# Kernel tuning notes

Hardware: AMD Instinct MI355X
Metric: run time of the kernel (lower is better)

## Reference

```python
import jax, jax.numpy as jnp
import numpy as np

N_NODES = 100000
EPS = 1e-5


def setup_inputs() -> dict:
    key = jax.random.key(0)
    ks = jax.random.split(key, 16)
    E_half = 1_600_000
    s = jax.random.randint(ks[0], (E_half,), 0, N_NODES, dtype=jnp.int32)
    d = jax.random.randint(ks[1], (E_half,), 0, N_NODES, dtype=jnp.int32)
    # bidirected graph, like dgl.to_bidirected
    src = jnp.concatenate([s, d])
    dst = jnp.concatenate([d, s])

    def glorot(k, i, o):
        lim = np.sqrt(6.0 / (i + o)).astype(np.float32)
        return jax.random.uniform(k, (i, o), jnp.float32, -lim, lim)

    return {
        "x": jax.random.normal(ks[2], (N_NODES, 128), jnp.float32),
        "src": src,
        "dst": dst,
        "W1": glorot(ks[3], 128, 256), "b1": jnp.zeros((256,), jnp.float32),
        "gamma1": jnp.ones((256,), jnp.float32), "beta1": jnp.zeros((256,), jnp.float32),
        "W2": glorot(ks[4], 256, 256), "b2": jnp.zeros((256,), jnp.float32),
        "gamma2": jnp.ones((256,), jnp.float32), "beta2": jnp.zeros((256,), jnp.float32),
        "W3": glorot(ks[5], 256, 40), "b3": jnp.zeros((40,), jnp.float32),
    }


def _graph_conv(x, src, dst, norm, W, b):
    # DGL GraphConv norm='both': h = D^{-1/2} A D^{-1/2} (x) W + b
    # project first when it shrinks the feature dim (matches DGL's ordering trick)
    if W.shape[0] > W.shape[1]:
        x = x @ W
        h = x * norm[:, None]
        m = jax.ops.segment_sum(h[src], dst, num_segments=N_NODES)
        return m * norm[:, None] + b
    h = x * norm[:, None]
    m = jax.ops.segment_sum(h[src], dst, num_segments=N_NODES)
    return (m * norm[:, None]) @ W + b


def _bn(h, gamma, beta):
    # BatchNorm1d in training mode: batch statistics over nodes, biased variance
    mean = jnp.mean(h, axis=0)
    var = jnp.var(h, axis=0)
    return (h - mean) * jax.lax.rsqrt(var + EPS) * gamma + beta


def reference(x, src, dst, W1, b1, gamma1, beta1, W2, b2, gamma2, beta2, W3, b3):
    # symmetric degrees (graph is bidirected), clamp min 1 like DGL
    deg = jax.ops.segment_sum(jnp.ones_like(dst, dtype=jnp.float32), dst,
                              num_segments=N_NODES)
    norm = jax.lax.rsqrt(jnp.maximum(deg, 1.0))

    h = _graph_conv(x, src, dst, norm, W1, b1)
    h = jax.nn.relu(_bn(h, gamma1, beta1))
    h = _graph_conv(h, src, dst, norm, W2, b2)
    h = jax.nn.relu(_bn(h, gamma2, beta2))
    h = _graph_conv(h, src, dst, norm, W3, b3)
    return jax.nn.log_softmax(h, axis=-1)
```

## Files before the change

kernel.cpp:

```cpp
#include <hip/hip_runtime.h>
#include <cstdint>
#include <cstddef>

#define NN 100000
#define BN_EPS 1e-5f

#define NB_SHIFT 7
#define NBUCK ((NN >> NB_SHIFT) + 1)
#define BSLOT 6400
#define T1_EPT 16
#define T1_TILE (256*T1_EPT)

typedef __attribute__((ext_vector_type(8))) short short8;
typedef __attribute__((ext_vector_type(4))) float f32x4;
typedef __attribute__((ext_vector_type(2))) float f32x2;

static __device__ __forceinline__ float bflo(unsigned u){ return __uint_as_float(u<<16); }
static __device__ __forceinline__ float bfhi(unsigned u){ return __uint_as_float(u & 0xFFFF0000u); }
static __device__ __forceinline__ unsigned short f2bf(float f){
  unsigned u = __float_as_uint(f);
  u += 0x7FFFu + ((u>>16)&1u);
  return (unsigned short)(u>>16);
}
static __device__ __forceinline__ unsigned pk2(float a, float b){
  return (unsigned)f2bf(a) | ((unsigned)f2bf(b) << 16);
}


__global__ __launch_bounds__(256) void k_b1(const int* __restrict__ src,
    const int* __restrict__ dst, int* __restrict__ bcnt,
    int* __restrict__ epairs, int E){
  __shared__ int hist[NBUCK];
  int tid = threadIdx.x;
  for(int j=tid; j<NBUCK; j+=256) hist[j]=0;
  __syncthreads();
  int base = blockIdx.x*T1_TILE;
  int pk[T1_EPT], bk[T1_EPT], r[T1_EPT];
  #pragma unroll
  for(int i=0;i<T1_EPT;i++){
    int e = base + i*256 + tid;
    if(e<E){
      int s=src[e], d=dst[e];
      bk[i]=d>>NB_SHIFT;
      pk[i]= s | ((d&127)<<20);
      r[i]=atomicAdd(&hist[bk[i]], 1);
    }
  }
  __syncthreads();
  for(int j=tid; j<NBUCK; j+=256){
    int h = hist[j];
    if(h>0) hist[j] = atomicAdd(&bcnt[j*16], h);
  }
  __syncthreads();
  #pragma unroll
  for(int i=0;i<T1_EPT;i++){
    int e = base + i*256 + tid;
    if(e<E) epairs[(size_t)bk[i]*BSLOT + hist[bk[i]] + r[i]] = pk[i];
  }
}

__global__ __launch_bounds__(256) void k_b2a(const int* __restrict__ epairs,
    const int* __restrict__ bcnt, float* __restrict__ norm, int* __restrict__ deg,
    int* __restrict__ ptot){
  __shared__ int h[128];
  int b = blockIdx.x, tid = threadIdx.x;
  if(tid<128) h[tid]=0;
  __syncthreads();
  int c = bcnt[b*16];
  const int* ep = epairs + (size_t)b*BSLOT;
  for(int j=tid; j<c; j+=256) atomicAdd(&h[ep[j]>>20], 1);
  __syncthreads();
  int n0 = b<<NB_SHIFT, nmax = min(128, NN-n0);
  if(tid<nmax){
    norm[n0+tid] = rsqrtf(fmaxf((float)h[tid], 1.0f));
    deg[n0+tid] = h[tid];
  }
  if(tid<64){
    int p0=(h[2*tid]+7)&~7, p1=(h[2*tid+1]+7)&~7;
    int s=p0+p1;
    #pragma unroll
    for(int off=1; off<64; off<<=1) s += __shfl_xor(s, off, 64);
    if(tid==0) ptot[b]=s;
  }
}

__global__ __launch_bounds__(1024) void k_scanB(const int* __restrict__ ptot,
    int* __restrict__ bbase, int* __restrict__ rp, float* __restrict__ norm){
  __shared__ int sm[1024];
  int t = threadIdx.x;
  int v = (t<NBUCK)? ptot[t] : 0;
  sm[t]=v; __syncthreads();
  for(int off=1; off<1024; off<<=1){
    int u = (t>=off)? sm[t-off] : 0;
    __syncthreads();
    sm[t]+=u;
    __syncthreads();
  }
  if(t<NBUCK) bbase[t] = sm[t]-v;
  if(t==NBUCK-1){ bbase[NBUCK]=sm[t]; rp[NN]=sm[t]; }
  if(t==0) norm[NN]=0.f;
}

__global__ __launch_bounds__(256) void k_b2b(const int* __restrict__ epairs,
    const int* __restrict__ bcnt, const int* __restrict__ bbase,
    const int* __restrict__ deg, int* __restrict__ rp, int* __restrict__ esrc){
  __shared__ int h[128];
  __shared__ int loc[129];
  int b = blockIdx.x, tid = threadIdx.x;
  int n0 = b<<NB_SHIFT, nmax = min(128, NN-n0);
  if(tid<128) h[tid] = (tid<nmax) ? deg[n0+tid] : 0;
  __syncthreads();
  if(tid<64){
    int p0=(h[2*tid]+7)&~7, p1=(h[2*tid+1]+7)&~7;
    int s=p0+p1;
    #pragma unroll
    for(int off=1; off<64; off<<=1){ int u=__shfl_up(s, off, 64); if(tid>=off) s+=u; }
    loc[2*tid]   = s-p0-p1;
    loc[2*tid+1] = s-p1;
    if(tid==63) loc[128]=s;
  }
  __syncthreads();
  int base = bbase[b];
  if(tid<nmax) rp[n0+tid] = base + loc[tid];
  if(tid<128) h[tid] = base + loc[tid];
  __syncthreads();
  int c = bcnt[b*16];
  const int* ep = epairs + (size_t)b*BSLOT;
  for(int j=tid; j<c; j+=256){
    int p = ep[j];
    int pos = atomicAdd(&h[p>>20], 1);
    esrc[pos] = p & 0xFFFFF;
  }
  __syncthreads();
  for(int i=tid; i<nmax; i+=256){
    int end = base + loc[i+1];
    for(int j=h[i]; j<end; j++) esrc[j]=NN;
  }
}

#define PB_W1 1
#define PB_W2 129
#define PB_W3 385
#define PB_SX 449
#define PB_END (PB_SX + 6250)

__global__ __launch_bounds__(256) void k_prep(
    const float* __restrict__ W1, const float* __restrict__ W2, const float* __restrict__ W3,
    const float* __restrict__ x, const float* __restrict__ norm,
    unsigned short* __restrict__ Wt1, unsigned short* __restrict__ Wt2,
    unsigned short* __restrict__ Wt3, unsigned char* __restrict__ Hx8,
    unsigned short* __restrict__ X3p, unsigned short* __restrict__ Z){
  int bid = blockIdx.x, t = threadIdx.x;
  if(bid == 0){
    if(t<128) Hx8[(size_t)NN*128 + t] = 0;
    if(t<40)  X3p[(size_t)NN*64 + t] = 0;
    Z[(size_t)NN*256 + t] = 0;
  }else if(bid < PB_W2){
    int i = (bid-PB_W1)*256 + t;
    int k = i >> 8, n = i & 255;
    Wt1[(size_t)n*128 + k] = f2bf(W1[i]);
  }else if(bid < PB_W3){
    int i = (bid-PB_W2)*256 + t;
    int k = i >> 8, n = i & 255;
    Wt2[(size_t)n*256 + k] = f2bf(W2[i]);
  }else if(bid < PB_SX){
    int i = (bid-PB_W3)*256 + t;
    int n = i >> 8, k = i & 255;
    Wt3[i] = (n < 40) ? f2bf(W3[(size_t)k*40 + n]) : (unsigned short)0;
  }else{
    int i = (bid-PB_SX)*256 + t;
    float4 v0 = *(const float4*)(x + (size_t)i*8);
    float4 v1 = *(const float4*)(x + (size_t)i*8 + 4);
    float nn = norm[i>>4];
    int p0 = __builtin_amdgcn_cvt_pk_fp8_f32(v0.x*nn, v0.y*nn, 0, false);
    p0     = __builtin_amdgcn_cvt_pk_fp8_f32(v0.z*nn, v0.w*nn, p0, true);
    int p1 = __builtin_amdgcn_cvt_pk_fp8_f32(v1.x*nn, v1.y*nn, 0, false);
    p1     = __builtin_amdgcn_cvt_pk_fp8_f32(v1.z*nn, v1.w*nn, p1, true);
    uint2 w; w.x = (unsigned)p0; w.y = (unsigned)p1;
    *(uint2*)(Hx8 + (size_t)i*8) = w;
  }
}


__global__ __launch_bounds__(256) void k_bnrelu8(const unsigned short* __restrict__ Z,
    const float* __restrict__ sums, const float* __restrict__ gamma,
    const float* __restrict__ beta, const float* __restrict__ norm,
    unsigned char* __restrict__ H8, int total4){
  __shared__ float s_sc[256], s_sh[256];
  int t = threadIdx.x;
  {
    float mean = sums[t]*(1.0f/NN);
    float var  = sums[256+t]*(1.0f/NN) - mean*mean;
    float sc = gamma[t]*rsqrtf(var + BN_EPS);
    s_sc[t] = sc;
    s_sh[t] = beta[t] - mean*sc;
  }
  __syncthreads();
  int i = blockIdx.x*blockDim.x + t;
  if(i<total4){
    int c8 = (i & 31) * 8;
    float nn = norm[i>>5];
    uint4 v = *(const uint4*)(Z + (size_t)i*8);
    float4 sc0 = *(const float4*)(s_sc + c8);
    float4 sc1 = *(const float4*)(s_sc + c8 + 4);
    float4 sh0 = *(const float4*)(s_sh + c8);
    float4 sh1 = *(const float4*)(s_sh + c8 + 4);
    float f0 = fmaxf(bflo(v.x)*sc0.x+sh0.x,0.f)*nn;
    float f1 = fmaxf(bfhi(v.x)*sc0.y+sh0.y,0.f)*nn;
    float f2 = fmaxf(bflo(v.y)*sc0.z+sh0.z,0.f)*nn;
    float f3 = fmaxf(bfhi(v.y)*sc0.w+sh0.w,0.f)*nn;
    float f4 = fmaxf(bflo(v.z)*sc1.x+sh1.x,0.f)*nn;
    float f5 = fmaxf(bfhi(v.z)*sc1.y+sh1.y,0.f)*nn;
    float f6 = fmaxf(bflo(v.w)*sc1.z+sh1.z,0.f)*nn;
    float f7 = fmaxf(bfhi(v.w)*sc1.w+sh1.w,0.f)*nn;
    int p0 = __builtin_amdgcn_cvt_pk_fp8_f32(f0, f1, 0, false);
    p0     = __builtin_amdgcn_cvt_pk_fp8_f32(f2, f3, p0, true);
    int p1 = __builtin_amdgcn_cvt_pk_fp8_f32(f4, f5, 0, false);
    p1     = __builtin_amdgcn_cvt_pk_fp8_f32(f6, f7, p1, true);
    uint2 w; w.x = (unsigned)p0; w.y = (unsigned)p1;
    *(uint2*)(H8 + (size_t)i*8) = w;
  }
}


__global__ __launch_bounds__(64) void k_agg128f8(const unsigned char* __restrict__ H,
    const int* __restrict__ rp, const int* __restrict__ esrc,
    const float* __restrict__ norm, unsigned short* __restrict__ out){
  int node = blockIdx.x, lane = threadIdx.x;
  int s0 = rp[node], s1 = rp[node+1];
  int g = lane >> 3, c = lane & 7;
  f32x2 av[8] = {};
  for(int e=s0; e<s1; e+=8){
    int4 A4 = *(const int4*)(esrc+e);
    int4 B4 = *(const int4*)(esrc+e+4);
    int idx = g<4 ? (g==0?A4.x: g==1?A4.y: g==2?A4.z: A4.w)
                  : (g==4?B4.x: g==5?B4.y: g==6?B4.z: B4.w);
    uint4 v = *(const uint4*)(H + (size_t)idx*128 + c*16);
    av[0] += __builtin_amdgcn_cvt_pk_f32_fp8((int)v.x, false);
    av[1] += __builtin_amdgcn_cvt_pk_f32_fp8((int)v.x, true );
    av[2] += __builtin_amdgcn_cvt_pk_f32_fp8((int)v.y, false);
    av[3] += __builtin_amdgcn_cvt_pk_f32_fp8((int)v.y, true );
    av[4] += __builtin_amdgcn_cvt_pk_f32_fp8((int)v.z, false);
    av[5] += __builtin_amdgcn_cvt_pk_f32_fp8((int)v.z, true );
    av[6] += __builtin_amdgcn_cvt_pk_f32_fp8((int)v.w, false);
    av[7] += __builtin_amdgcn_cvt_pk_f32_fp8((int)v.w, true );
  }
  #pragma unroll
  for(int off=8; off<64; off<<=1){
    #pragma unroll
    for(int j=0;j<8;j++){
      av[j][0] += __shfl_xor(av[j][0], off, 64);
      av[j][1] += __shfl_xor(av[j][1], off, 64);
    }
  }
  if(g==0){
    float nn = norm[node];
    uint4 w0, w1;
    w0.x = pk2(av[0][0]*nn, av[0][1]*nn); w0.y = pk2(av[1][0]*nn, av[1][1]*nn);
    w0.z = pk2(av[2][0]*nn, av[2][1]*nn); w0.w = pk2(av[3][0]*nn, av[3][1]*nn);
    w1.x = pk2(av[4][0]*nn, av[4][1]*nn); w1.y = pk2(av[5][0]*nn, av[5][1]*nn);
    w1.z = pk2(av[6][0]*nn, av[6][1]*nn); w1.w = pk2(av[7][0]*nn, av[7][1]*nn);
    unsigned short* o = out + (size_t)node*128 + c*16;
    *(uint4*)o = w0;
    *(uint4*)(o+8) = w1;
  }
}

__global__ __launch_bounds__(64) void k_agg256h(const unsigned char* __restrict__ H,
    const int* __restrict__ rp, const int* __restrict__ esrc,
    const float* __restrict__ norm, unsigned short* __restrict__ out){
  int bid = blockIdx.x;
  int half = bid & 1, node = bid >> 1;
  int lane = threadIdx.x;
  int s0 = rp[node], s1 = rp[node+1];
  int g = lane >> 3, c = lane & 7;
  const unsigned char* Hh = H + half*128;
  f32x2 av[8] = {};
  for(int e=s0; e<s1; e+=8){
    int4 A4 = *(const int4*)(esrc+e);
    int4 B4 = *(const int4*)(esrc+e+4);
    int idx = g<4 ? (g==0?A4.x: g==1?A4.y: g==2?A4.z: A4.w)
                  : (g==4?B4.x: g==5?B4.y: g==6?B4.z: B4.w);
    uint4 v = *(const uint4*)(Hh + (size_t)idx*256 + c*16);
    av[0] += __builtin_amdgcn_cvt_pk_f32_fp8((int)v.x, false);
    av[1] += __builtin_amdgcn_cvt_pk_f32_fp8((int)v.x, true );
    av[2] += __builtin_amdgcn_cvt_pk_f32_fp8((int)v.y, false);
    av[3] += __builtin_amdgcn_cvt_pk_f32_fp8((int)v.y, true );
    av[4] += __builtin_amdgcn_cvt_pk_f32_fp8((int)v.z, false);
    av[5] += __builtin_amdgcn_cvt_pk_f32_fp8((int)v.z, true );
    av[6] += __builtin_amdgcn_cvt_pk_f32_fp8((int)v.w, false);
    av[7] += __builtin_amdgcn_cvt_pk_f32_fp8((int)v.w, true );
  }
  #pragma unroll
  for(int off=8; off<64; off<<=1){
    #pragma unroll
    for(int j=0;j<8;j++){
      av[j][0] += __shfl_xor(av[j][0], off, 64);
      av[j][1] += __shfl_xor(av[j][1], off, 64);
    }
  }
  if(g==0){
    float nn = norm[node];
    uint4 w0, w1;
    w0.x = pk2(av[0][0]*nn, av[0][1]*nn); w0.y = pk2(av[1][0]*nn, av[1][1]*nn);
    w0.z = pk2(av[2][0]*nn, av[2][1]*nn); w0.w = pk2(av[3][0]*nn, av[3][1]*nn);
    w1.x = pk2(av[4][0]*nn, av[4][1]*nn); w1.y = pk2(av[5][0]*nn, av[5][1]*nn);
    w1.z = pk2(av[6][0]*nn, av[6][1]*nn); w1.w = pk2(av[7][0]*nn, av[7][1]*nn);
    unsigned short* o = out + (size_t)node*256 + half*128 + c*16;
    *(uint4*)o = w0;
    *(uint4*)(o+8) = w1;
  }
}

__global__ __launch_bounds__(64) void k_agg64(const unsigned short* __restrict__ X3p,
    const int* __restrict__ rp, const int* __restrict__ esrc,
    const float* __restrict__ norm, const float* __restrict__ b3,
    float* __restrict__ out){
  int node = blockIdx.x, lane = threadIdx.x;
  int s0 = rp[node], s1 = rp[node+1];
  int es = lane >> 3, s = lane & 7;
  float a[8] = {};
  for(int e=s0; e<s1; e+=8){
    int4 A4 = *(const int4*)(esrc+e);
    int4 B4 = *(const int4*)(esrc+e+4);
    int idx = es==0?A4.x: es==1?A4.y: es==2?A4.z: es==3?A4.w:
              es==4?B4.x: es==5?B4.y: es==6?B4.z: B4.w;
    if(s<5){
      uint4 v = *(const uint4*)(X3p + (size_t)idx*64 + s*8);
      a[0]+=bflo(v.x); a[1]+=bfhi(v.x); a[2]+=bflo(v.y); a[3]+=bfhi(v.y);
      a[4]+=bflo(v.z); a[5]+=bfhi(v.z); a[6]+=bflo(v.w); a[7]+=bfhi(v.w);
    }
  }
  #pragma unroll
  for(int off=8; off<64; off<<=1){
    #pragma unroll
    for(int j=0;j<8;j++) a[j] += __shfl_xor(a[j], off, 64);
  }
  bool act = s < 5;
  float nn = norm[node];
  float bv[8] = {};
  if(act){
    float4 t0 = *(const float4*)(b3 + s*8);
    float4 t1 = *(const float4*)(b3 + s*8 + 4);
    bv[0]=t0.x; bv[1]=t0.y; bv[2]=t0.z; bv[3]=t0.w;
    bv[4]=t1.x; bv[5]=t1.y; bv[6]=t1.z; bv[7]=t1.w;
  }
  float v[8];
  float mx = -INFINITY;
  #pragma unroll
  for(int j=0;j<8;j++){
    v[j] = act ? (a[j]*nn + bv[j]) : -INFINITY;
    mx = fmaxf(mx, v[j]);
  }
  #pragma unroll
  for(int off=32; off; off>>=1) mx = fmaxf(mx, __shfl_xor(mx, off, 64));
  float sum = 0.f;
  if(act && es==0){
    #pragma unroll
    for(int j=0;j<8;j++) sum += expf(v[j]-mx);
  }
  #pragma unroll
  for(int off=32; off; off>>=1) sum += __shfl_xor(sum, off, 64);
  float lse = logf(sum);
  if(act && es==0){
    float4 o0, o1;
    o0.x=v[0]-mx-lse; o0.y=v[1]-mx-lse; o0.z=v[2]-mx-lse; o0.w=v[3]-mx-lse;
    o1.x=v[4]-mx-lse; o1.y=v[5]-mx-lse; o1.z=v[6]-mx-lse; o1.w=v[7]-mx-lse;
    *(float4*)(out + (size_t)node*40 + s*8) = o0;
    *(float4*)(out + (size_t)node*40 + s*8 + 4) = o1;
  }
}


__global__ __launch_bounds__(256) void k_mgemm(
    const unsigned short* __restrict__ A, const unsigned short* __restrict__ Bt,
    const float* __restrict__ bias, unsigned short* __restrict__ C,
    float* __restrict__ sums, int M, int K, int Nn){
  __shared__ unsigned short As[128*64];
  __shared__ unsigned short Bs[128*64];
  int nt = Nn >> 7;
  int bm = blockIdx.x / nt, bn = blockIdx.x % nt;
  int m0 = bm*128, n0 = bn*128;
  int tid = threadIdx.x;
  int wave = tid >> 6, lane = tid & 63;
  int wm = (wave>>1)*64, wn = (wave&1)*64;
  int lrow = lane & 15, lq = lane >> 4;
  int srow = lane >> 3;
  int sx = ((lane & 7) ^ srow) * 8;
  f32x4 acc[4][4] = {};
  for(int k0=0; k0<K; k0+=64){
    __syncthreads();
    #pragma unroll
    for(int c4=0;c4<4;c4++){
      int c = wave*4 + c4;
      int grow = c*8 + srow;
      const unsigned short* ga = A + (size_t)(m0+grow)*K + k0 + sx;
      __builtin_amdgcn_global_load_lds((const __attribute__((address_space(1))) void*)ga,
          (__attribute__((address_space(3))) void*)(As + (size_t)c*512), 16, 0, 0);
      const unsigned short* gb = Bt + (size_t)(n0+grow)*K + k0 + sx;
      __builtin_amdgcn_global_load_lds((const __attribute__((address_space(1))) void*)gb,
          (__attribute__((address_space(3))) void*)(Bs + (size_t)c*512), 16, 0, 0);
    }
    __syncthreads();
    #pragma unroll
    for(int kk=0;kk<2;kk++){
      short8 af[4], bf[4];
      #pragma unroll
      for(int i=0;i<4;i++){
        int Ra = wm + i*16 + lrow;
        int ca = (kk*4 + lq) ^ (Ra & 7);
        af[i] = *(const short8*)(As + Ra*64 + ca*8);
        int Rb = wn + i*16 + lrow;
        int cb = (kk*4 + lq) ^ (Rb & 7);
        bf[i] = *(const short8*)(Bs + Rb*64 + cb*8);
      }
      #pragma unroll
      for(int i=0;i<4;i++)
        #pragma unroll
        for(int j=0;j<4;j++)
          acc[i][j] = __builtin_amdgcn_mfma_f32_16x16x32_bf16(af[i], bf[j], acc[i][j], 0, 0, 0);
    }
  }
  #pragma unroll
  for(int j=0;j<4;j++){
    int col = n0 + wn + j*16 + lrow;
    float bj = bias[col];
    float s=0.f, s2=0.f;
    #pragma unroll
    for(int i=0;i<4;i++){
      #pragma unroll
      for(int r=0;r<4;r++){
        int row = m0 + wm + i*16 + lq*4 + r;
        if(row < M){
          float v = acc[i][j][r] + bj;
          s += v; s2 += v*v;
          C[(size_t)row*Nn + col] = f2bf(v);
        }
      }
    }
    s  += __shfl_xor(s, 16, 64);  s  += __shfl_xor(s, 32, 64);
    s2 += __shfl_xor(s2, 16, 64); s2 += __shfl_xor(s2, 32, 64);
    if(lq == 0){
      atomicAdd(&sums[col], s);
      atomicAdd(&sums[256+col], s2);
    }
  }
}

__global__ __launch_bounds__(256) void k_mgemm3(
    const unsigned short* __restrict__ Zin, const unsigned short* __restrict__ Bt,
    const float* __restrict__ sums, const float* __restrict__ gamma,
    const float* __restrict__ beta, const float* __restrict__ rownorm,
    unsigned short* __restrict__ X3p, int M, int K){
  __shared__ unsigned short As[128*64];
  __shared__ unsigned short Bs[64*64];
  __shared__ float s_sc[256], s_sh[256];
  int m0 = blockIdx.x*128;
  int tid = threadIdx.x;
  {
    float mean = sums[tid]*(1.0f/NN);
    float var  = sums[256+tid]*(1.0f/NN) - mean*mean;
    float sc = gamma[tid]*rsqrtf(var + BN_EPS);
    s_sc[tid] = sc;
    s_sh[tid] = beta[tid] - mean*sc;
  }
  __syncthreads();
  int wave = tid >> 6, lane = tid & 63;
  int wm = wave*32;
  int lrow = lane & 15, lq = lane >> 4;
  int srow = lane >> 3;
  int sx = ((lane & 7) ^ srow) * 8;
  f32x4 acc[2][4] = {};
  for(int k0=0; k0<K; k0+=64){
    uint4 raw[4];
    #pragma unroll
    for(int c4=0;c4<4;c4++){
      int c = wave*4 + c4;
      int grow = c*8 + srow;
      raw[c4] = *(const uint4*)(Zin + (size_t)(m0+grow)*K + k0 + sx);
    }
    float4 sc0 = *(const float4*)(s_sc + k0 + sx);
    float4 sc1 = *(const float4*)(s_sc + k0 + sx + 4);
    float4 sh0 = *(const float4*)(s_sh + k0 + sx);
    float4 sh1 = *(const float4*)(s_sh + k0 + sx + 4);
    __syncthreads();
    #pragma unroll
    for(int c4=0;c4<4;c4++){
      int c = wave*4 + c4;
      uint4 w;
      w.x = pk2(fmaxf(bflo(raw[c4].x)*sc0.x+sh0.x,0.f), fmaxf(bfhi(raw[c4].x)*sc0.y+sh0.y,0.f));
      w.y = pk2(fmaxf(bflo(raw[c4].y)*sc0.z+sh0.z,0.f), fmaxf(bfhi(raw[c4].y)*sc0.w+sh0.w,0.f));
      w.z = pk2(fmaxf(bflo(raw[c4].z)*sc1.x+sh1.x,0.f), fmaxf(bfhi(raw[c4].z)*sc1.y+sh1.y,0.f));
      w.w = pk2(fmaxf(bflo(raw[c4].w)*sc1.z+sh1.z,0.f), fmaxf(bfhi(raw[c4].w)*sc1.w+sh1.w,0.f));
      *(uint4*)(As + (size_t)c*512 + (size_t)lane*8) = w;
    }
    #pragma unroll
    for(int c4=0;c4<2;c4++){
      int c = wave*2 + c4;
      int grow = c*8 + srow;
      const unsigned short* gb = Bt + (size_t)grow*K + k0 + sx;
      __builtin_amdgcn_global_load_lds((const __attribute__((address_space(1))) void*)gb,
          (__attribute__((address_space(3))) void*)(Bs + (size_t)c*512), 16, 0, 0);
    }
    __syncthreads();
    #pragma unroll
    for(int kk=0;kk<2;kk++){
      short8 af[2], bf[4];
      #pragma unroll
      for(int i=0;i<2;i++){
        int Ra = wm + i*16 + lrow;
        int ca = (kk*4 + lq) ^ (Ra & 7);
        af[i] = *(const short8*)(As + Ra*64 + ca*8);
      }
      #pragma unroll
      for(int j=0;j<4;j++){
        int Rb = j*16 + lrow;
        int cb = (kk*4 + lq) ^ (Rb & 7);
        bf[j] = *(const short8*)(Bs + Rb*64 + cb*8);
      }
      #pragma unroll
      for(int i=0;i<2;i++)
        #pragma unroll
        for(int j=0;j<4;j++)
          acc[i][j] = __builtin_amdgcn_mfma_f32_16x16x32_bf16(af[i], bf[j], acc[i][j], 0, 0, 0);
    }
  }
  #pragma unroll
  for(int j=0;j<4;j++){
    int col = j*16 + lrow;
    if(col < 40){
      #pragma unroll
      for(int i=0;i<2;i++){
        #pragma unroll
        for(int r=0;r<4;r++){
          int row = m0 + wm + i*16 + lq*4 + r;
          if(row < M) X3p[(size_t)row*64 + col] = f2bf(acc[i][j][r] * rownorm[row]);
        }
      }
    }
  }
}


extern "C" void kernel_launch(void* const* d_in, const int* in_sizes, int n_in,
                              void* d_out, int out_size, void* d_ws, size_t ws_size,
                              hipStream_t stream){
  const float* x   = (const float*)d_in[0];
  const int*   src = (const int*)d_in[1];
  const int*   dst = (const int*)d_in[2];
  const float* W1  = (const float*)d_in[3];
  const float* b1  = (const float*)d_in[4];
  const float* g1  = (const float*)d_in[5];
  const float* be1 = (const float*)d_in[6];
  const float* W2  = (const float*)d_in[7];
  const float* b2  = (const float*)d_in[8];
  const float* g2  = (const float*)d_in[9];
  const float* be2 = (const float*)d_in[10];
  const float* W3  = (const float*)d_in[11];
  const float* b3  = (const float*)d_in[12];
  float* out = (float*)d_out;
  const int N = NN;
  const int E = in_sizes[1];

  char* p = (char*)d_ws;
  size_t off = 0;
  auto alloc = [&](size_t bytes)->void*{
    void* r = p + off;
    off += (bytes + 511) & ~(size_t)511;
    return r;
  };
  int*   bcnt  = (int*)  alloc((size_t)NBUCK*16*4);
  float* sums1 = (float*)alloc(2048);
  float* sums2 = (float*)alloc(2048);
  size_t zero_bytes = off;
  int*   rp    = (int*)  alloc((size_t)(N+1)*4);
  float* norm  = (float*)alloc((size_t)(N+1)*4);
  int*   deg   = (int*)  alloc((size_t)N*4);
  int*   ptot  = (int*)  alloc((size_t)NBUCK*4);
  int*   bbase = (int*)  alloc((size_t)(NBUCK+1)*4);
  unsigned short* Wt1 = (unsigned short*)alloc((size_t)256*128*2);
  unsigned short* Wt2 = (unsigned short*)alloc((size_t)256*256*2);
  unsigned short* Wt3 = (unsigned short*)alloc((size_t)64*256*2);
  int*   esrc  = (int*)  alloc((size_t)(E + 7*N + 16)*4);
  unsigned short* Hx  = (unsigned short*)alloc((size_t)(N+1)*128*2);
  unsigned short* M1  = (unsigned short*)alloc((size_t)N*128*2);
  unsigned short* Mb2 = (unsigned short*)alloc((size_t)N*256*2);
  unsigned short* Z   = (unsigned short*)alloc((size_t)(N+1)*256*2);
  unsigned short* X3p = (unsigned short*)alloc((size_t)(N+1)*64*2);
  int* epairs = (int*)Mb2;
  unsigned char* Hx8 = (unsigned char*)Hx;
  unsigned char* H8  = (unsigned char*)Hx;
  (void)ws_size; (void)n_in; (void)out_size;

  hipMemsetAsync(d_ws, 0, zero_bytes, stream);

  k_b1    <<<(E+T1_TILE-1)/T1_TILE,256,0,stream>>>(src, dst, bcnt, epairs, E);
  k_b2a   <<<NBUCK,256,0,stream>>>(epairs, bcnt, norm, deg, ptot);
  k_scanB <<<1,1024,0,stream>>>(ptot, bbase, rp, norm);
  k_b2b   <<<NBUCK,256,0,stream>>>(epairs, bcnt, bbase, deg, rp, esrc);
  k_prep  <<<PB_END,256,0,stream>>>(W1, W2, W3, x, norm, Wt1, Wt2, Wt3, Hx8, X3p, Z);

  k_agg128f8<<<N,64,0,stream>>>(Hx8, rp, esrc, norm, M1);
  k_mgemm  <<<((N+127)/128)*2,256,0,stream>>>(M1, Wt1, b1, Z, sums1, N, 128, 256);

  k_bnrelu8<<<((N+1)*32+255)/256,256,0,stream>>>(Z, sums1, g1, be1, norm, H8, (N+1)*32);
  k_agg256h<<<2*N,64,0,stream>>>(H8, rp, esrc, norm, Mb2);
  k_mgemm  <<<((N+127)/128)*2,256,0,stream>>>(Mb2, Wt2, b2, Z, sums2, N, 256, 256);

  k_mgemm3 <<<(N+127)/128,256,0,stream>>>(Z, Wt3, sums2, g2, be2, norm, X3p, N, 256);
  k_agg64  <<<N,64,0,stream>>>(X3p, rp, esrc, norm, b3, out);
}
```

Baseline: 695.2 us.

## Slice fp8 feature tables into 32-byte column slabs for cache-local gathers

Stores the fp8 node-feature tables as separate 32-column slabs, each of size (N+1)*32 bytes, instead of row-major rows. One generic aggregation kernel replaces the two before it. Each wavefront gathers 16 neighbors at a time, with 8-byte loads per lane, for one slab, and each 256-thread block handles four nodes. Processing one slab at a time shrinks the working set each gather sweep touches, so it fits better in L2/MALL. The cost is more passes over the edge lists, since they are re-read once per slab, and smaller per-lane loads.

```diff
diff --git a/kernel.cpp b/kernel.cpp
--- a/kernel.cpp
+++ b/kernel.cpp
@@ -10,6 +10,8 @@
 #define BSLOT 6400
 #define T1_EPT 16
 #define T1_TILE (256*T1_EPT)
+
+#define SL_STRIDE ((size_t)(NN+1)*32)
 
 typedef __attribute__((ext_vector_type(8))) short short8;
 typedef __attribute__((ext_vector_type(4))) float f32x4;
@@ -152,7 +154,7 @@
     unsigned short* __restrict__ X3p, unsigned short* __restrict__ Z){
   int bid = blockIdx.x, t = threadIdx.x;
   if(bid == 0){
-    if(t<128) Hx8[(size_t)NN*128 + t] = 0;
+    if(t<128) Hx8[(size_t)(t>>5)*SL_STRIDE + (size_t)NN*32 + (t&31)] = 0;
     if(t<40)  X3p[(size_t)NN*64 + t] = 0;
     Z[(size_t)NN*256 + t] = 0;
   }else if(bid < PB_W2){
@@ -171,13 +173,14 @@
     int i = (bid-PB_SX)*256 + t;
     float4 v0 = *(const float4*)(x + (size_t)i*8);
     float4 v1 = *(const float4*)(x + (size_t)i*8 + 4);
-    float nn = norm[i>>4];
+    int row = i >> 4, q = i & 15;
+    float nn = norm[row];
     int p0 = __builtin_amdgcn_cvt_pk_fp8_f32(v0.x*nn, v0.y*nn, 0, false);
     p0     = __builtin_amdgcn_cvt_pk_fp8_f32(v0.z*nn, v0.w*nn, p0, true);
     int p1 = __builtin_amdgcn_cvt_pk_fp8_f32(v1.x*nn, v1.y*nn, 0, false);
     p1     = __builtin_amdgcn_cvt_pk_fp8_f32(v1.z*nn, v1.w*nn, p1, true);
     uint2 w; w.x = (unsigned)p0; w.y = (unsigned)p1;
-    *(uint2*)(Hx8 + (size_t)i*8) = w;
+    *(uint2*)(Hx8 + (size_t)(q>>2)*SL_STRIDE + (size_t)row*32 + (q&3)*8) = w;
   }
 }
 
@@ -198,8 +201,10 @@
   __syncthreads();
   int i = blockIdx.x*blockDim.x + t;
   if(i<total4){
-    int c8 = (i & 31) * 8;
-    float nn = norm[i>>5];
+    int q = i & 31;
+    int row = i >> 5;
+    int c8 = q * 8;
+    float nn = norm[row];
     uint4 v = *(const uint4*)(Z + (size_t)i*8);
     float4 sc0 = *(const float4*)(s_sc + c8);
     float4 sc1 = *(const float4*)(s_sc + c8 + 4);
@@ -218,97 +223,54 @@
     int p1 = __builtin_amdgcn_cvt_pk_fp8_f32(f4, f5, 0, false);
     p1     = __builtin_amdgcn_cvt_pk_fp8_f32(f6, f7, p1, true);
     uint2 w; w.x = (unsigned)p0; w.y = (unsigned)p1;
-    *(uint2*)(H8 + (size_t)i*8) = w;
-  }
-}
-
-
-__global__ __launch_bounds__(64) void k_agg128f8(const unsigned char* __restrict__ H,
+    *(uint2*)(H8 + (size_t)(q>>2)*SL_STRIDE + (size_t)row*32 + (q&3)*8) = w;
+  }
+}
+
+__global__ __launch_bounds__(256) void k_aggs(const unsigned char* __restrict__ H,
     const int* __restrict__ rp, const int* __restrict__ esrc,
-    const float* __restrict__ norm, unsigned short* __restrict__ out){
-  int node = blockIdx.x, lane = threadIdx.x;
+    const float* __restrict__ norm, unsigned short* __restrict__ out,
+    int sShift, int outStride){
+  int bid = blockIdx.x;
+  int sMask = (1<<sShift)-1;
+  int s = bid & sMask;
+  int node = ((bid >> sShift)<<2) + (threadIdx.x>>6);
+  int lane = threadIdx.x & 63;
+  const unsigned char* Hs = H + (size_t)s*SL_STRIDE;
   int s0 = rp[node], s1 = rp[node+1];
-  int g = lane >> 3, c = lane & 7;
-  f32x2 av[8] = {};
-  for(int e=s0; e<s1; e+=8){
+  int g = lane >> 2, c = lane & 3;
+  f32x2 av[4] = {};
+  for(int e=s0; e<s1; e+=16){
     int4 A4 = *(const int4*)(esrc+e);
     int4 B4 = *(const int4*)(esrc+e+4);
-    int idx = g<4 ? (g==0?A4.x: g==1?A4.y: g==2?A4.z: A4.w)
-                  : (g==4?B4.x: g==5?B4.y: g==6?B4.z: B4.w);
-    uint4 v = *(const uint4*)(H + (size_t)idx*128 + c*16);
+    bool more = (e+8 < s1);
+    int4 C4 = more ? *(const int4*)(esrc+e+8)  : make_int4(NN,NN,NN,NN);
+    int4 D4 = more ? *(const int4*)(esrc+e+12) : make_int4(NN,NN,NN,NN);
+    int4 Q = (g<4)?A4 : (g<8)?B4 : (g<12)?C4 : D4;
+    int sel = g & 3;
+    int idx = sel==0?Q.x: sel==1?Q.y: sel==2?Q.z: Q.w;
+    uint2 v = *(const uint2*)(Hs + (size_t)idx*32 + c*8);
     av[0] += __builtin_amdgcn_cvt_pk_f32_fp8((int)v.x, false);
     av[1] += __builtin_amdgcn_cvt_pk_f32_fp8((int)v.x, true );
     av[2] += __builtin_amdgcn_cvt_pk_f32_fp8((int)v.y, false);
     av[3] += __builtin_amdgcn_cvt_pk_f32_fp8((int)v.y, true );
-    av[4] += __builtin_amdgcn_cvt_pk_f32_fp8((int)v.z, false);
-    av[5] += __builtin_amdgcn_cvt_pk_f32_fp8((int)v.z, true );
-    av[6] += __builtin_amdgcn_cvt_pk_f32_fp8((int)v.w, false);
-    av[7] += __builtin_amdgcn_cvt_pk_f32_fp8((int)v.w, true );
-  }
-  #pragma unroll
-  for(int off=8; off<64; off<<=1){
-    #pragma unroll
-    for(int j=0;j<8;j++){
+  }
+  #pragma unroll
+  for(int off=4; off<64; off<<=1){
+    #pragma unroll
+    for(int j=0;j<4;j++){
       av[j][0] += __shfl_xor(av[j][0], off, 64);
       av[j][1] += __shfl_xor(av[j][1], off, 64);
     }
   }
   if(g==0){
     float nn = norm[node];
-    uint4 w0, w1;
-    w0.x = pk2(av[0][0]*nn, av[0][1]*nn); w0.y = pk2(av[1][0]*nn, av[1][1]*nn);
-    w0.z = pk2(av[2][0]*nn, av[2][1]*nn); w0.w = pk2(av[3][0]*nn, av[3][1]*nn);
-    w1.x = pk2(av[4][0]*nn, av[4][1]*nn); w1.y = pk2(av[5][0]*nn, av[5][1]*nn);
-    w1.z = pk2(av[6][0]*nn, av[6][1]*nn); w1.w = pk2(av[7][0]*nn, av[7][1]*nn);
-    unsigned short* o = out + (size_t)node*128 + c*16;
-    *(uint4*)o = w0;
-    *(uint4*)(o+8) = w1;
-  }
-}
-
-__global__ __launch_bounds__(64) void k_agg256h(const unsigned char* __restrict__ H,
-    const int* __restrict__ rp, const int* __restrict__ esrc,
-    const float* __restrict__ norm, unsigned short* __restrict__ out){
-  int bid = blockIdx.x;
-  int half = bid & 1, node = bid >> 1;
-  int lane = threadIdx.x;
-  int s0 = rp[node], s1 = rp[node+1];
-  int g = lane >> 3, c = lane & 7;
-  const unsigned char* Hh = H + half*128;
-  f32x2 av[8] = {};
-  for(int e=s0; e<s1; e+=8){
-    int4 A4 = *(const int4*)(esrc+e);
-    int4 B4 = *(const int4*)(esrc+e+4);
-    int idx = g<4 ? (g==0?A4.x: g==1?A4.y: g==2?A4.z: A4.w)
-                  : (g==4?B4.x: g==5?B4.y: g==6?B4.z: B4.w);
-    uint4 v = *(const uint4*)(Hh + (size_t)idx*256 + c*16);
-    av[0] += __builtin_amdgcn_cvt_pk_f32_fp8((int)v.x, false);
-    av[1] += __builtin_amdgcn_cvt_pk_f32_fp8((int)v.x, true );
-    av[2] += __builtin_amdgcn_cvt_pk_f32_fp8((int)v.y, false);
-    av[3] += __builtin_amdgcn_cvt_pk_f32_fp8((int)v.y, true );
-    av[4] += __builtin_amdgcn_cvt_pk_f32_fp8((int)v.z, false);
-    av[5] += __builtin_amdgcn_cvt_pk_f32_fp8((int)v.z, true );
-    av[6] += __builtin_amdgcn_cvt_pk_f32_fp8((int)v.w, false);
-    av[7] += __builtin_amdgcn_cvt_pk_f32_fp8((int)v.w, true );
-  }
-  #pragma unroll
-  for(int off=8; off<64; off<<=1){
-    #pragma unroll
-    for(int j=0;j<8;j++){
-      av[j][0] += __shfl_xor(av[j][0], off, 64);
-      av[j][1] += __shfl_xor(av[j][1], off, 64);
-    }
-  }
-  if(g==0){
-    float nn = norm[node];
-    uint4 w0, w1;
-    w0.x = pk2(av[0][0]*nn, av[0][1]*nn); w0.y = pk2(av[1][0]*nn, av[1][1]*nn);
-    w0.z = pk2(av[2][0]*nn, av[2][1]*nn); w0.w = pk2(av[3][0]*nn, av[3][1]*nn);
-    w1.x = pk2(av[4][0]*nn, av[4][1]*nn); w1.y = pk2(av[5][0]*nn, av[5][1]*nn);
-    w1.z = pk2(av[6][0]*nn, av[6][1]*nn); w1.w = pk2(av[7][0]*nn, av[7][1]*nn);
-    unsigned short* o = out + (size_t)node*256 + half*128 + c*16;
-    *(uint4*)o = w0;
-    *(uint4*)(o+8) = w1;
+    uint4 w;
+    w.x = pk2(av[0][0]*nn, av[0][1]*nn);
+    w.y = pk2(av[1][0]*nn, av[1][1]*nn);
+    w.z = pk2(av[2][0]*nn, av[2][1]*nn);
+    w.w = pk2(av[3][0]*nn, av[3][1]*nn);
+    *(uint4*)(out + (size_t)node*outStride + s*32 + c*8) = w;
   }
 }
 
@@ -600,12 +562,12 @@
   k_b2b   <<<NBUCK,256,0,stream>>>(epairs, bcnt, bbase, deg, rp, esrc);
   k_prep  <<<PB_END,256,0,stream>>>(W1, W2, W3, x, norm, Wt1, Wt2, Wt3, Hx8, X3p, Z);
 
-  k_agg128f8<<<N,64,0,stream>>>(Hx8, rp, esrc, norm, M1);
-  k_mgemm  <<<((N+127)/128)*2,256,0,stream>>>(M1, Wt1, b1, Z, sums1, N, 128, 256);
+  k_aggs  <<<(N/4)*4,256,0,stream>>>(Hx8, rp, esrc, norm, M1, 2, 128);
+  k_mgemm <<<((N+127)/128)*2,256,0,stream>>>(M1, Wt1, b1, Z, sums1, N, 128, 256);
 
   k_bnrelu8<<<((N+1)*32+255)/256,256,0,stream>>>(Z, sums1, g1, be1, norm, H8, (N+1)*32);
-  k_agg256h<<<2*N,64,0,stream>>>(H8, rp, esrc, norm, Mb2);
-  k_mgemm  <<<((N+127)/128)*2,256,0,stream>>>(Mb2, Wt2, b2, Z, sums2, N, 256, 256);
+  k_aggs  <<<(N/4)*8,256,0,stream>>>(H8, rp, esrc, norm, Mb2, 3, 256);
+  k_mgemm <<<((N+127)/128)*2,256,0,stream>>>(Mb2, Wt2, b2, Z, sums2, N, 256, 256);
 
   k_mgemm3 <<<(N+127)/128,256,0,stream>>>(Z, Wt3, sums2, g2, be2, norm, X3p, N, 256);
   k_agg64  <<<N,64,0,stream>>>(X3p, rp, esrc, norm, b3, out);
```

New measurement: 1.026 ms. +47.6%, slower.
